# Optimization experiments

Hardware: AMD Instinct MI355X
Metric: run time of the kernel (lower is better)

The kernel has to match this reference:

```python
import jax, jax.numpy as jnp
import numpy as np

EPS = 1e-12  # matches torch F.normalize eps

def _l2norm(v, axis):
    n = jnp.sqrt(jnp.sum(v * v, axis=axis, keepdims=True))
    return v / jnp.maximum(n, EPS)

def setup_inputs() -> dict:
    key = jax.random.key(0)
    k1, k2, k3 = jax.random.split(key, 3)
    N, D, H, W, K = 64, 128, 60, 80, 64
    x = jax.random.normal(k1, (N, D, H, W), dtype=jnp.float32)
    conv_w = jax.random.normal(k2, (K, D), dtype=jnp.float32) * 0.1
    centroids = jax.random.uniform(k3, (K, D), dtype=jnp.float32)
    return {"x": x, "conv_w": conv_w, "centroids": centroids}

def reference(x, conv_w, centroids):
    N, D, H, W = x.shape
    K = conv_w.shape[0]
    # descriptor-wise L2 normalization over channel dim
    x = _l2norm(x, axis=1)
    xf = x.reshape(N, D, H * W)                       # [N, D, P]
    # 1x1 conv (no bias) == matmul over channels, then softmax over clusters
    logits = jnp.einsum('kd,ndp->nkp', conv_w, xf)    # [N, K, P]
    sa = jax.nn.softmax(logits, axis=1)               # [N, K, P]
    # vlad[n,k,:] = sum_p sa[n,k,p] * (xf[n,:,p] - centroids[k])
    agg = jnp.einsum('nkp,ndp->nkd', sa, xf)          # [N, K, D]
    vlad = agg - sa.sum(axis=-1)[..., None] * centroids[None]
    vlad = _l2norm(vlad, axis=2)                      # intra-normalization
    vlad = vlad.reshape(N, K * D)
    vlad = _l2norm(vlad, axis=1)                      # global L2 norm
    return vlad
```

## Files before the change

kernel.cpp:

```cpp
#include <hip/hip_runtime.h>
#include <hip/hip_bf16.h>
#include <math.h>

#define NN 64
#define DD 128
#define PP 4800
#define KK 64
#define BPN 15
#define PB  320
#define CP  64
#define NCH 5

#define WT  136
#define XPT 136
#define XDT 72
#define SAT 72

#define PAGG_SZ  ((size_t)NN * BPN * KK * DD)
#define PSSUM_SZ ((size_t)NN * BPN * KK)
#define VTMP_SZ  ((size_t)NN * KK * DD)
#define GSUM_SZ  ((size_t)NN * 8)

typedef __attribute__((ext_vector_type(8))) short bf16x8;
typedef __attribute__((ext_vector_type(4))) float f32x4;

__device__ __forceinline__ unsigned short f2bf(float f) {
  unsigned u = __float_as_uint(f);
  u += 0x7fffu + ((u >> 16) & 1u);
  return (unsigned short)(u >> 16);
}
__device__ __forceinline__ unsigned pk2(float a, float b) {
  union { __hip_bfloat162 h2; unsigned u; } cv;
  cv.h2 = __float22bfloat162_rn(make_float2(a, b));
  return cv.u;
}

__global__ __launch_bounds__(256, 2) void main_kernel(const float* __restrict__ x,
                                                      const float* __restrict__ conv_w,
                                                      float* __restrict__ pagg,
                                                      float* __restrict__ pssum) {
  __shared__ __align__(16) unsigned short w_s[KK * WT];
  __shared__ __align__(16) unsigned short xpd[CP * XPT];
  __shared__ __align__(16) unsigned short xdp[DD * XDT];
  __shared__ __align__(16) unsigned short sa_s[KK * SAT];
  __shared__ float red_s[256];

  const int b = blockIdx.x;
  const int n = b / BPN, sl = b % BPN;
  const int t = threadIdx.x, lane = t & 63, wv = t >> 6;
  const int lq = lane >> 4, ll = lane & 15;
  const int pb = t & 7, db = t >> 3;

  {
    int k = t >> 2, h = t & 3;
    const float* wp = conv_w + k * DD + h * 32;
    unsigned short* dst = &w_s[k * WT + h * 32];
#pragma unroll
    for (int i = 0; i < 4; ++i) {
      float4 a = *(const float4*)(wp + 8 * i);
      float4 c = *(const float4*)(wp + 8 * i + 4);
      uint4 o = {pk2(a.x, a.y), pk2(a.z, a.w), pk2(c.x, c.y), pk2(c.z, c.w)};
      *(uint4*)&dst[8 * i] = o;
    }
  }
  if (t < 64) red_s[t] = 0.f;

  const float* xb = x + (size_t)n * DD * PP + (size_t)(4 * db) * PP + sl * PB + 8 * pb;

  float4 pf[8];
#pragma unroll
  for (int r = 0; r < 4; ++r) {
    pf[2 * r]     = *(const float4*)(xb + (size_t)r * PP);
    pf[2 * r + 1] = *(const float4*)(xb + (size_t)r * PP + 4);
  }

  f32x4 acc[8];
#pragma unroll
  for (int i = 0; i < 8; ++i) acc[i] = (f32x4){0.f, 0.f, 0.f, 0.f};
  float ssacc[16];
#pragma unroll
  for (int i = 0; i < 16; ++i) ssacc[i] = 0.f;

  for (int c = 0; c < NCH; ++c) {
    float4 cur[8];
#pragma unroll
    for (int i = 0; i < 8; ++i) cur[i] = pf[i];
    if (c + 1 < NCH) {
      const float* xc = xb + (c + 1) * CP;
#pragma unroll
      for (int r = 0; r < 4; ++r) {
        pf[2 * r]     = *(const float4*)(xc + (size_t)r * PP);
        pf[2 * r + 1] = *(const float4*)(xc + (size_t)r * PP + 4);
      }
    }

    float sq[8];
#pragma unroll
    for (int h = 0; h < 2; ++h)
#pragma unroll
      for (int j = 0; j < 4; ++j) {
        float s = 0.f;
#pragma unroll
        for (int r = 0; r < 4; ++r) {
          float v = (&cur[2 * r + h].x)[j];
          s = fmaf(v, v, s);
        }
        sq[4 * h + j] = s;
      }
#pragma unroll
    for (int i = 0; i < 8; ++i) {
      sq[i] += __shfl_xor(sq[i], 8);
      sq[i] += __shfl_xor(sq[i], 16);
      sq[i] += __shfl_xor(sq[i], 32);
    }

    __syncthreads();

    if (lane < 8) {
#pragma unroll
      for (int j = 0; j < 8; ++j) atomicAdd(&red_s[8 * lane + j], sq[j]);
    }

    {
      unsigned prow[4][4];
#pragma unroll
      for (int r = 0; r < 4; ++r) {
        const float4& a = cur[2 * r];
        const float4& c2 = cur[2 * r + 1];
        prow[r][0] = pk2(a.x, a.y);
        prow[r][1] = pk2(a.z, a.w);
        prow[r][2] = pk2(c2.x, c2.y);
        prow[r][3] = pk2(c2.z, c2.w);
        uint4 o = {prow[r][0], prow[r][1], prow[r][2], prow[r][3]};
        *(uint4*)&xdp[(4 * db + r) * XDT + 8 * pb] = o;
      }
      const int colh = (((db >> 1) ^ pb) << 3) + (db & 1) * 4;
#pragma unroll
      for (int j2 = 0; j2 < 4; ++j2) {
        unsigned lo01 = __builtin_amdgcn_perm(prow[1][j2], prow[0][j2], 0x05040100u);
        unsigned hi01 = __builtin_amdgcn_perm(prow[1][j2], prow[0][j2], 0x07060302u);
        unsigned lo23 = __builtin_amdgcn_perm(prow[3][j2], prow[2][j2], 0x05040100u);
        unsigned hi23 = __builtin_amdgcn_perm(prow[3][j2], prow[2][j2], 0x07060302u);
        int p_e = 8 * pb + 2 * j2;
        *(uint2*)&xpd[p_e * XPT + colh]       = make_uint2(lo01, lo23);
        *(uint2*)&xpd[(p_e + 1) * XPT + colh] = make_uint2(hi01, hi23);
      }
    }
    __syncthreads();

    {
      const int prow_ = wv * 16 + ll;
      const int swz = (2 * wv + (ll >> 3)) & 7;
      f32x4 lg[4];
#pragma unroll
      for (int kt = 0; kt < 4; ++kt) lg[kt] = (f32x4){0.f, 0.f, 0.f, 0.f};
#pragma unroll
      for (int ks = 0; ks < 4; ++ks) {
        bf16x8 bfrag = *(const bf16x8*)&xpd[prow_ * XPT + ((((ks << 2) | lq) ^ swz) << 3)];
#pragma unroll
        for (int kt = 0; kt < 4; ++kt) {
          bf16x8 afrag = *(const bf16x8*)&w_s[(kt * 16 + ll) * WT + ks * 32 + lq * 8];
          lg[kt] = __builtin_amdgcn_mfma_f32_16x16x32_bf16(afrag, bfrag, lg[kt], 0, 0, 0);
        }
      }
      float iv = 1.0f / fmaxf(sqrtf(red_s[prow_]), 1e-12f);
      float vals[16];
      float m = -1e30f;
#pragma unroll
      for (int kt = 0; kt < 4; ++kt)
#pragma unroll
        for (int r = 0; r < 4; ++r) {
          float v = lg[kt][r] * iv;
          vals[kt * 4 + r] = v;
          m = fmaxf(m, v);
        }
      m = fmaxf(m, __shfl_xor(m, 16));
      m = fmaxf(m, __shfl_xor(m, 32));
      float se = 0.f;
#pragma unroll
      for (int i = 0; i < 16; ++i) {
        float e = __expf(vals[i] - m);
        vals[i] = e;
        se += e;
      }
      se += __shfl_xor(se, 16);
      se += __shfl_xor(se, 32);
      float rinv = 1.0f / se;
      float r2 = rinv * iv;
#pragma unroll
      for (int kt = 0; kt < 4; ++kt)
#pragma unroll
        for (int r = 0; r < 4; ++r) {
          float e = vals[kt * 4 + r];
          ssacc[kt * 4 + r] += e * rinv;
          sa_s[(kt * 16 + lq * 4 + r) * SAT + prow_] = f2bf(e * r2);
        }
    }
    __syncthreads();
    if (c + 1 < NCH && t < 64) red_s[t] = 0.f;

#pragma unroll
    for (int ks = 0; ks < 2; ++ks) {
      bf16x8 afrag = *(const bf16x8*)&sa_s[(wv * 16 + ll) * SAT + ks * 32 + lq * 8];
#pragma unroll
      for (int dt = 0; dt < 8; ++dt) {
        bf16x8 bfrag = *(const bf16x8*)&xdp[(dt * 16 + ll) * XDT + ks * 32 + lq * 8];
        acc[dt] = __builtin_amdgcn_mfma_f32_16x16x32_bf16(afrag, bfrag, acc[dt], 0, 0, 0);
      }
    }
  }

  {
    float* base = pagg + (size_t)(n * BPN + sl) * (KK * DD);
#pragma unroll
    for (int dt = 0; dt < 8; ++dt)
#pragma unroll
      for (int r = 0; r < 4; ++r)
        base[(16 * wv + 4 * lq + r) * DD + dt * 16 + ll] = acc[dt][r];
  }
#pragma unroll
  for (int i = 0; i < 16; ++i) {
    float s = ssacc[i];
    s += __shfl_xor(s, 1);
    s += __shfl_xor(s, 2);
    s += __shfl_xor(s, 4);
    s += __shfl_xor(s, 8);
    if (ll == 0) red_s[wv * 64 + (i >> 2) * 16 + lq * 4 + (i & 3)] = s;
  }
  __syncthreads();
  if (t < 64)
    pssum[(n * BPN + sl) * KK + t] =
        red_s[t] + red_s[64 + t] + red_s[128 + t] + red_s[192 + t];
}

__global__ __launch_bounds__(256) void ep1_kernel(const float* __restrict__ pagg,
                                                  const float* __restrict__ pssum,
                                                  const float* __restrict__ cent,
                                                  float* __restrict__ vtmp,
                                                  float* __restrict__ gsum) {
  __shared__ float wsum[4];
  const int blk = blockIdx.x;
  const int n = blk >> 3, kg = blk & 7;
  const int t = threadIdx.x;
  const int kl = t >> 5, c32 = t & 31;
  const int k = kg * 8 + kl;
  const size_t off = (size_t)k * DD + c32 * 4;

  const float* base = pagg + (size_t)n * BPN * (KK * DD) + off;
  float4 a = {0.f, 0.f, 0.f, 0.f};
  for (int s = 0; s < BPN; ++s) {
    float4 v = *(const float4*)(base + (size_t)s * (KK * DD));
    a.x += v.x; a.y += v.y; a.z += v.z; a.w += v.w;
  }
  float sk = 0.f;
  for (int s = 0; s < BPN; ++s) sk += pssum[(n * BPN + s) * KK + k];

  float4 c4 = *(const float4*)(cent + off);
  float4 v;
  v.x = fmaf(-sk, c4.x, a.x);
  v.y = fmaf(-sk, c4.y, a.y);
  v.z = fmaf(-sk, c4.z, a.z);
  v.w = fmaf(-sk, c4.w, a.w);

  float pss = v.x * v.x + v.y * v.y + v.z * v.z + v.w * v.w;
  float ss = pss;
  ss += __shfl_xor(ss, 1);
  ss += __shfl_xor(ss, 2);
  ss += __shfl_xor(ss, 4);
  ss += __shfl_xor(ss, 8);
  ss += __shfl_xor(ss, 16);
  float rinv = 1.0f / fmaxf(sqrtf(ss), 1e-12f);
  v.x *= rinv; v.y *= rinv; v.z *= rinv; v.w *= rinv;
  *(float4*)(vtmp + (size_t)n * (KK * DD) + off) = v;

  float gp = pss * rinv * rinv;
#pragma unroll
  for (int o = 1; o < 64; o <<= 1) gp += __shfl_xor(gp, o);
  if ((t & 63) == 0) wsum[t >> 6] = gp;
  __syncthreads();
  if (t == 0) gsum[blk] = wsum[0] + wsum[1] + wsum[2] + wsum[3];
}

__global__ __launch_bounds__(256) void ep2_kernel(const float* __restrict__ vtmp,
                                                  const float* __restrict__ gsum,
                                                  float* __restrict__ out) {
  const int n = blockIdx.x, t = threadIdx.x;
  const float* gs = gsum + n * 8;
  float g = gs[0] + gs[1] + gs[2] + gs[3] + gs[4] + gs[5] + gs[6] + gs[7];
  float ginv = 1.0f / fmaxf(sqrtf(g), 1e-12f);
  const float4* vi = (const float4*)(vtmp + (size_t)n * (KK * DD));
  float4* vo = (float4*)(out + (size_t)n * (KK * DD));
#pragma unroll
  for (int it = 0; it < 8; ++it) {
    int idx = t + 256 * it;
    float4 f = vi[idx];
    f.x *= ginv; f.y *= ginv; f.z *= ginv; f.w *= ginv;
    vo[idx] = f;
  }
}

extern "C" void kernel_launch(void* const* d_in, const int* in_sizes, int n_in,
                              void* d_out, int out_size, void* d_ws, size_t ws_size,
                              hipStream_t stream) {
  const float* x      = (const float*)d_in[0];
  const float* conv_w = (const float*)d_in[1];
  const float* cent   = (const float*)d_in[2];
  float* out = (float*)d_out;
  float* ws  = (float*)d_ws;

  float* pagg  = ws;
  float* pssum = pagg + PAGG_SZ;
  float* vtmp  = pssum + PSSUM_SZ;
  float* gsum  = vtmp + VTMP_SZ;

  main_kernel<<<NN * BPN, 256, 0, stream>>>(x, conv_w, pagg, pssum);
  ep1_kernel<<<NN * 8, 256, 0, stream>>>(pagg, pssum, cent, vtmp, gsum);
  ep2_kernel<<<NN, 256, 0, stream>>>(vtmp, gsum, out);
}
```

Measured before the change: 246.8 us.

## Fuse epilogue kernels into main kernel via last-block ticket reduction

Replaces the two epilogue kernel launches with a per-sample atomic ticket, so the last of the 15 slice blocks for each sample sums the partial aggregates, applies the centroid correction and both L2 normalizations, and writes the output. This removes two launches and the vtmp/gsum round trips through global memory. In exchange it adds a memset launch, fences and atomics, and a serial tail in which one block per sample does all the reduction work. Shared memory is merged into a single aliased buffer so the epilogue can reuse it.

```diff
diff --git a/kernel.cpp b/kernel.cpp
--- a/kernel.cpp
+++ b/kernel.cpp
@@ -18,8 +18,17 @@
 
 #define PAGG_SZ  ((size_t)NN * BPN * KK * DD)
 #define PSSUM_SZ ((size_t)NN * BPN * KK)
-#define VTMP_SZ  ((size_t)NN * KK * DD)
-#define GSUM_SZ  ((size_t)NN * 8)
+
+#define SM_W    0
+#define SM_XPD  17408
+#define SM_XDP  34816
+#define SM_SA   53248
+#define SM_RED  62464
+#define SM_TOT  63488
+#define SM_AGG  0
+#define SM_SRED 33792
+#define SM_WSUM 34048
+#define SM_FLAG 34064
 
 typedef __attribute__((ext_vector_type(8))) short bf16x8;
 typedef __attribute__((ext_vector_type(4))) float f32x4;
@@ -37,13 +46,17 @@
 
 __global__ __launch_bounds__(256, 2) void main_kernel(const float* __restrict__ x,
                                                       const float* __restrict__ conv_w,
+                                                      const float* __restrict__ cent,
                                                       float* __restrict__ pagg,
-                                                      float* __restrict__ pssum) {
-  __shared__ __align__(16) unsigned short w_s[KK * WT];
-  __shared__ __align__(16) unsigned short xpd[CP * XPT];
-  __shared__ __align__(16) unsigned short xdp[DD * XDT];
-  __shared__ __align__(16) unsigned short sa_s[KK * SAT];
-  __shared__ float red_s[256];
+                                                      float* __restrict__ pssum,
+                                                      int* __restrict__ tickets,
+                                                      float* __restrict__ out) {
+  __shared__ __align__(16) unsigned char smem[SM_TOT];
+  unsigned short* w_s  = (unsigned short*)(smem + SM_W);
+  unsigned short* xpd  = (unsigned short*)(smem + SM_XPD);
+  unsigned short* xdp  = (unsigned short*)(smem + SM_XDP);
+  unsigned short* sa_s = (unsigned short*)(smem + SM_SA);
+  float*          red_s = (float*)(smem + SM_RED);
 
   const int b = blockIdx.x;
   const int n = b / BPN, sl = b % BPN;
@@ -218,6 +231,7 @@
       for (int r = 0; r < 4; ++r)
         base[(16 * wv + 4 * lq + r) * DD + dt * 16 + ll] = acc[dt][r];
   }
+  __syncthreads();
 #pragma unroll
   for (int i = 0; i < 16; ++i) {
     float s = ssacc[i];
@@ -231,71 +245,90 @@
   if (t < 64)
     pssum[(n * BPN + sl) * KK + t] =
         red_s[t] + red_s[64 + t] + red_s[128 + t] + red_s[192 + t];
-}
-
-__global__ __launch_bounds__(256) void ep1_kernel(const float* __restrict__ pagg,
-                                                  const float* __restrict__ pssum,
-                                                  const float* __restrict__ cent,
-                                                  float* __restrict__ vtmp,
-                                                  float* __restrict__ gsum) {
-  __shared__ float wsum[4];
-  const int blk = blockIdx.x;
-  const int n = blk >> 3, kg = blk & 7;
-  const int t = threadIdx.x;
-  const int kl = t >> 5, c32 = t & 31;
-  const int k = kg * 8 + kl;
-  const size_t off = (size_t)k * DD + c32 * 4;
-
-  const float* base = pagg + (size_t)n * BPN * (KK * DD) + off;
-  float4 a = {0.f, 0.f, 0.f, 0.f};
-  for (int s = 0; s < BPN; ++s) {
-    float4 v = *(const float4*)(base + (size_t)s * (KK * DD));
-    a.x += v.x; a.y += v.y; a.z += v.z; a.w += v.w;
-  }
-  float sk = 0.f;
-  for (int s = 0; s < BPN; ++s) sk += pssum[(n * BPN + s) * KK + k];
-
-  float4 c4 = *(const float4*)(cent + off);
-  float4 v;
-  v.x = fmaf(-sk, c4.x, a.x);
-  v.y = fmaf(-sk, c4.y, a.y);
-  v.z = fmaf(-sk, c4.z, a.z);
-  v.w = fmaf(-sk, c4.w, a.w);
-
-  float pss = v.x * v.x + v.y * v.y + v.z * v.z + v.w * v.w;
-  float ss = pss;
-  ss += __shfl_xor(ss, 1);
-  ss += __shfl_xor(ss, 2);
-  ss += __shfl_xor(ss, 4);
-  ss += __shfl_xor(ss, 8);
-  ss += __shfl_xor(ss, 16);
-  float rinv = 1.0f / fmaxf(sqrtf(ss), 1e-12f);
-  v.x *= rinv; v.y *= rinv; v.z *= rinv; v.w *= rinv;
-  *(float4*)(vtmp + (size_t)n * (KK * DD) + off) = v;
-
-  float gp = pss * rinv * rinv;
-#pragma unroll
-  for (int o = 1; o < 64; o <<= 1) gp += __shfl_xor(gp, o);
-  if ((t & 63) == 0) wsum[t >> 6] = gp;
-  __syncthreads();
-  if (t == 0) gsum[blk] = wsum[0] + wsum[1] + wsum[2] + wsum[3];
-}
-
-__global__ __launch_bounds__(256) void ep2_kernel(const float* __restrict__ vtmp,
-                                                  const float* __restrict__ gsum,
-                                                  float* __restrict__ out) {
-  const int n = blockIdx.x, t = threadIdx.x;
-  const float* gs = gsum + n * 8;
-  float g = gs[0] + gs[1] + gs[2] + gs[3] + gs[4] + gs[5] + gs[6] + gs[7];
-  float ginv = 1.0f / fmaxf(sqrtf(g), 1e-12f);
-  const float4* vi = (const float4*)(vtmp + (size_t)n * (KK * DD));
-  float4* vo = (float4*)(out + (size_t)n * (KK * DD));
+
+  __threadfence();
+  __syncthreads();
+  int* flag = (int*)(smem + SM_FLAG);
+  if (t == 0) {
+    int prev = atomicAdd(&tickets[n], 1);
+    *flag = (prev == BPN - 1) ? 1 : 0;
+  }
+  __syncthreads();
+  if (*flag == 0) return;
+  __threadfence();
+
+  float* agg_s = (float*)(smem + SM_AGG);
+  float* sred  = (float*)(smem + SM_SRED);
+  float* wsum  = (float*)(smem + SM_WSUM);
+  __syncthreads();
+
 #pragma unroll
   for (int it = 0; it < 8; ++it) {
     int idx = t + 256 * it;
-    float4 f = vi[idx];
-    f.x *= ginv; f.y *= ginv; f.z *= ginv; f.w *= ginv;
-    vo[idx] = f;
+    float4 a = {0.f, 0.f, 0.f, 0.f};
+    const float4* base = (const float4*)(pagg + (size_t)n * BPN * (KK * DD));
+    for (int s = 0; s < BPN; ++s) {
+      float4 v = base[(size_t)s * (KK * DD / 4) + idx];
+      a.x += v.x; a.y += v.y; a.z += v.z; a.w += v.w;
+    }
+    int row = idx >> 5, col = (idx & 31) * 4;
+    *(float4*)&agg_s[row * 132 + col] = a;
+  }
+  if (t < KK) {
+    float s = 0.f;
+    for (int ss = 0; ss < BPN; ++ss) s += pssum[(n * BPN + ss) * KK + t];
+    sred[t] = s;
+  }
+  __syncthreads();
+
+  {
+    const int k = t >> 2, j = t & 3;
+    const float* ap = &agg_s[k * 132 + 32 * j];
+    const float* cp = cent + (size_t)k * DD + 32 * j;
+    const float sk = sred[k];
+
+    float v[32];
+    float ss = 0.f;
+#pragma unroll
+    for (int i = 0; i < 32; i += 4) {
+      float4 a4 = *(const float4*)(ap + i);
+      float4 c4 = *(const float4*)(cp + i);
+      v[i + 0] = fmaf(-sk, c4.x, a4.x);
+      v[i + 1] = fmaf(-sk, c4.y, a4.y);
+      v[i + 2] = fmaf(-sk, c4.z, a4.z);
+      v[i + 3] = fmaf(-sk, c4.w, a4.w);
+      ss = fmaf(v[i + 0], v[i + 0], ss);
+      ss = fmaf(v[i + 1], v[i + 1], ss);
+      ss = fmaf(v[i + 2], v[i + 2], ss);
+      ss = fmaf(v[i + 3], v[i + 3], ss);
+    }
+    ss += __shfl_xor(ss, 1);
+    ss += __shfl_xor(ss, 2);
+    float rinv = 1.0f / fmaxf(sqrtf(ss), 1e-12f);
+
+    float gp = 0.f;
+#pragma unroll
+    for (int i = 0; i < 32; ++i) {
+      v[i] *= rinv;
+      gp = fmaf(v[i], v[i], gp);
+    }
+#pragma unroll
+    for (int o = 1; o < 64; o <<= 1) gp += __shfl_xor(gp, o);
+    if ((t & 63) == 0) wsum[t >> 6] = gp;
+    __syncthreads();
+    float g = wsum[0] + wsum[1] + wsum[2] + wsum[3];
+    float ginv = 1.0f / fmaxf(sqrtf(g), 1e-12f);
+
+    float* op = out + (size_t)n * KK * DD + (size_t)k * DD + 32 * j;
+#pragma unroll
+    for (int i = 0; i < 32; i += 4) {
+      float4 o;
+      o.x = v[i + 0] * ginv;
+      o.y = v[i + 1] * ginv;
+      o.z = v[i + 2] * ginv;
+      o.w = v[i + 3] * ginv;
+      *(float4*)(op + i) = o;
+    }
   }
 }
 
@@ -310,10 +343,8 @@
 
   float* pagg  = ws;
   float* pssum = pagg + PAGG_SZ;
-  float* vtmp  = pssum + PSSUM_SZ;
-  float* gsum  = vtmp + VTMP_SZ;
-
-  main_kernel<<<NN * BPN, 256, 0, stream>>>(x, conv_w, pagg, pssum);
-  ep1_kernel<<<NN * 8, 256, 0, stream>>>(pagg, pssum, cent, vtmp, gsum);
-  ep2_kernel<<<NN, 256, 0, stream>>>(vtmp, gsum, out);
+  int* tickets = (int*)(pssum + PSSUM_SZ);
+
+  hipMemsetAsync(tickets, 0, NN * sizeof(int), stream);
+  main_kernel<<<NN * BPN, 256, 0, stream>>>(x, conv_w, cent, pagg, pssum, tickets, out);
 }
```

Result: slower. 461.2 us (+86.9%).

## Keep conv weights in registers, cut blocks per sample, raise occupancy to three

Applied to the files above, without the earlier changes.

Conv weight fragments now stay in registers instead of a shared-memory tile, which frees LDS and removes the per-chunk weight reads from shared memory. Blocks per sample drop from 15 to 12 with an uneven 7/6 chunk split, so each block amortises its setup and partial-aggregate write over more pixels and the partial buffers the epilogue reduces get smaller. Launch bounds go from 2 to 3 blocks per SM, and the next-chunk prefetch moves after the LDS stores to save registers. In exchange, register pressure rises from the held weight fragments and the work per block becomes slightly unbalanced.

```diff
diff --git a/kernel.cpp b/kernel.cpp
--- a/kernel.cpp
+++ b/kernel.cpp
@@ -6,12 +6,9 @@
 #define DD 128
 #define PP 4800
 #define KK 64
-#define BPN 15
-#define PB  320
+#define BPN 12
 #define CP  64
-#define NCH 5
-
-#define WT  136
+
 #define XPT 136
 #define XDT 72
 #define SAT 72
@@ -19,7 +16,6 @@
 #define PAGG_SZ  ((size_t)NN * BPN * KK * DD)
 #define PSSUM_SZ ((size_t)NN * BPN * KK)
 #define VTMP_SZ  ((size_t)NN * KK * DD)
-#define GSUM_SZ  ((size_t)NN * 8)
 
 typedef __attribute__((ext_vector_type(8))) short bf16x8;
 typedef __attribute__((ext_vector_type(4))) float f32x4;
@@ -34,44 +30,52 @@
   cv.h2 = __float22bfloat162_rn(make_float2(a, b));
   return cv.u;
 }
-
-__global__ __launch_bounds__(256, 2) void main_kernel(const float* __restrict__ x,
+__device__ __forceinline__ bf16x8 pk8(float4 a, float4 b) {
+  union { unsigned u[4]; bf16x8 v; } r;
+  r.u[0] = pk2(a.x, a.y);
+  r.u[1] = pk2(a.z, a.w);
+  r.u[2] = pk2(b.x, b.y);
+  r.u[3] = pk2(b.z, b.w);
+  return r.v;
+}
+
+__global__ __launch_bounds__(256, 3) void main_kernel(const float* __restrict__ x,
                                                       const float* __restrict__ conv_w,
                                                       float* __restrict__ pagg,
                                                       float* __restrict__ pssum) {
-  __shared__ __align__(16) unsigned short w_s[KK * WT];
-  __shared__ __align__(16) unsigned short xpd[CP * XPT];
+  __shared__ __align__(16) unsigned short xpd[KK * XPT];
   __shared__ __align__(16) unsigned short xdp[DD * XDT];
   __shared__ __align__(16) unsigned short sa_s[KK * SAT];
   __shared__ float red_s[256];
 
   const int b = blockIdx.x;
-  const int n = b / BPN, sl = b % BPN;
+  const int n = b / BPN, j = b % BPN;
+  const int cnt = (j < 3) ? 7 : 6;
+  const int ch0 = j * 6 + ((j < 3) ? j : 3);
   const int t = threadIdx.x, lane = t & 63, wv = t >> 6;
   const int lq = lane >> 4, ll = lane & 15;
   const int pb = t & 7, db = t >> 3;
 
-  {
-    int k = t >> 2, h = t & 3;
-    const float* wp = conv_w + k * DD + h * 32;
-    unsigned short* dst = &w_s[k * WT + h * 32];
-#pragma unroll
-    for (int i = 0; i < 4; ++i) {
-      float4 a = *(const float4*)(wp + 8 * i);
-      float4 c = *(const float4*)(wp + 8 * i + 4);
-      uint4 o = {pk2(a.x, a.y), pk2(a.z, a.w), pk2(c.x, c.y), pk2(c.z, c.w)};
-      *(uint4*)&dst[8 * i] = o;
+  bf16x8 wf[4][4];
+#pragma unroll
+  for (int kt = 0; kt < 4; ++kt) {
+    const float* wr = conv_w + (kt * 16 + ll) * DD + lq * 8;
+#pragma unroll
+    for (int ks = 0; ks < 4; ++ks) {
+      float4 a = *(const float4*)(wr + ks * 32);
+      float4 c = *(const float4*)(wr + ks * 32 + 4);
+      wf[kt][ks] = pk8(a, c);
     }
   }
   if (t < 64) red_s[t] = 0.f;
 
-  const float* xb = x + (size_t)n * DD * PP + (size_t)(4 * db) * PP + sl * PB + 8 * pb;
+  const float* xb = x + (size_t)n * DD * PP + (size_t)(4 * db) * PP + 8 * pb;
 
   float4 pf[8];
 #pragma unroll
   for (int r = 0; r < 4; ++r) {
-    pf[2 * r]     = *(const float4*)(xb + (size_t)r * PP);
-    pf[2 * r + 1] = *(const float4*)(xb + (size_t)r * PP + 4);
+    pf[2 * r]     = *(const float4*)(xb + (size_t)r * PP + ch0 * CP);
+    pf[2 * r + 1] = *(const float4*)(xb + (size_t)r * PP + ch0 * CP + 4);
   }
 
   f32x4 acc[8];
@@ -81,31 +85,19 @@
 #pragma unroll
   for (int i = 0; i < 16; ++i) ssacc[i] = 0.f;
 
-  for (int c = 0; c < NCH; ++c) {
-    float4 cur[8];
-#pragma unroll
-    for (int i = 0; i < 8; ++i) cur[i] = pf[i];
-    if (c + 1 < NCH) {
-      const float* xc = xb + (c + 1) * CP;
-#pragma unroll
-      for (int r = 0; r < 4; ++r) {
-        pf[2 * r]     = *(const float4*)(xc + (size_t)r * PP);
-        pf[2 * r + 1] = *(const float4*)(xc + (size_t)r * PP + 4);
-      }
-    }
-
+  for (int c = 0; c < cnt; ++c) {
     float sq[8];
 #pragma unroll
     for (int h = 0; h < 2; ++h)
 #pragma unroll
-      for (int j = 0; j < 4; ++j) {
+      for (int jj = 0; jj < 4; ++jj) {
         float s = 0.f;
 #pragma unroll
         for (int r = 0; r < 4; ++r) {
-          float v = (&cur[2 * r + h].x)[j];
+          float v = (&pf[2 * r + h].x)[jj];
           s = fmaf(v, v, s);
         }
-        sq[4 * h + j] = s;
+        sq[4 * h + jj] = s;
       }
 #pragma unroll
     for (int i = 0; i < 8; ++i) {
@@ -118,15 +110,15 @@
 
     if (lane < 8) {
 #pragma unroll
-      for (int j = 0; j < 8; ++j) atomicAdd(&red_s[8 * lane + j], sq[j]);
+      for (int jj = 0; jj < 8; ++jj) atomicAdd(&red_s[8 * lane + jj], sq[jj]);
     }
 
     {
       unsigned prow[4][4];
 #pragma unroll
       for (int r = 0; r < 4; ++r) {
-        const float4& a = cur[2 * r];
-        const float4& c2 = cur[2 * r + 1];
+        const float4& a = pf[2 * r];
+        const float4& c2 = pf[2 * r + 1];
         prow[r][0] = pk2(a.x, a.y);
         prow[r][1] = pk2(a.z, a.w);
         prow[r][2] = pk2(c2.x, c2.y);
@@ -146,6 +138,14 @@
         *(uint2*)&xpd[(p_e + 1) * XPT + colh] = make_uint2(hi01, hi23);
       }
     }
+    if (c + 1 < cnt) {
+      const float* xc = xb + (size_t)(ch0 + c + 1) * CP;
+#pragma unroll
+      for (int r = 0; r < 4; ++r) {
+        pf[2 * r]     = *(const float4*)(xc + (size_t)r * PP);
+        pf[2 * r + 1] = *(const float4*)(xc + (size_t)r * PP + 4);
+      }
+    }
     __syncthreads();
 
     {
@@ -158,10 +158,8 @@
       for (int ks = 0; ks < 4; ++ks) {
         bf16x8 bfrag = *(const bf16x8*)&xpd[prow_ * XPT + ((((ks << 2) | lq) ^ swz) << 3)];
 #pragma unroll
-        for (int kt = 0; kt < 4; ++kt) {
-          bf16x8 afrag = *(const bf16x8*)&w_s[(kt * 16 + ll) * WT + ks * 32 + lq * 8];
-          lg[kt] = __builtin_amdgcn_mfma_f32_16x16x32_bf16(afrag, bfrag, lg[kt], 0, 0, 0);
-        }
+        for (int kt = 0; kt < 4; ++kt)
+          lg[kt] = __builtin_amdgcn_mfma_f32_16x16x32_bf16(wf[kt][ks], bfrag, lg[kt], 0, 0, 0);
       }
       float iv = 1.0f / fmaxf(sqrtf(red_s[prow_]), 1e-12f);
       float vals[16];
@@ -197,7 +195,7 @@
         }
     }
     __syncthreads();
-    if (c + 1 < NCH && t < 64) red_s[t] = 0.f;
+    if (c + 1 < cnt && t < 64) red_s[t] = 0.f;
 
 #pragma unroll
     for (int ks = 0; ks < 2; ++ks) {
@@ -211,13 +209,14 @@
   }
 
   {
-    float* base = pagg + (size_t)(n * BPN + sl) * (KK * DD);
+    float* base = pagg + (size_t)(n * BPN + j) * (KK * DD);
 #pragma unroll
     for (int dt = 0; dt < 8; ++dt)
 #pragma unroll
       for (int r = 0; r < 4; ++r)
         base[(16 * wv + 4 * lq + r) * DD + dt * 16 + ll] = acc[dt][r];
   }
+  __syncthreads();
 #pragma unroll
   for (int i = 0; i < 16; ++i) {
     float s = ssacc[i];
@@ -229,7 +228,7 @@
   }
   __syncthreads();
   if (t < 64)
-    pssum[(n * BPN + sl) * KK + t] =
+    pssum[(n * BPN + j) * KK + t] =
         red_s[t] + red_s[64 + t] + red_s[128 + t] + red_s[192 + t];
 }
 
```

Measured after the change: 265.0 us. 7.4% more time.
